# Kernel optimization log

Measured on AMD Instinct MI355X. Metric: run time of the kernel, lower is better.

Reference implementation:

```python
import jax, jax.numpy as jnp
import numpy as np

H = 16        # num_heads
D = 128       # head_dim = hidden_size // num_heads
HID = 2048    # hidden_size
BLOCK = 64    # moba_chunk_size
TOPK = 8      # moba_topk


def setup_inputs() -> dict:
    key = jax.random.key(0)
    ks = jax.random.split(key, 5)
    B, S = 1, 2048
    hidden_states = jax.random.normal(ks[0], (B, S, HID), dtype=jnp.float32)
    scale = HID ** -0.5
    Wq = jax.random.normal(ks[1], (HID, H * D), dtype=jnp.float32) * scale
    Wk = jax.random.normal(ks[2], (HID, H * D), dtype=jnp.float32) * scale
    Wv = jax.random.normal(ks[3], (HID, H * D), dtype=jnp.float32) * scale
    Wo = jax.random.normal(ks[4], (H * D, HID), dtype=jnp.float32) * scale
    return {"hidden_states": hidden_states, "Wq": Wq, "Wk": Wk, "Wv": Wv, "Wo": Wo}


def _moba_forward(hidden_states, Wq, Wk, Wv, Wo):
    B, S, _ = hidden_states.shape
    nb = S // BLOCK
    INF = jnp.float32(jnp.inf)

    q = (hidden_states @ Wq).reshape(B, S, H, D)
    k = (hidden_states @ Wk).reshape(B, S, H, D)
    v = (hidden_states @ Wv).reshape(B, S, H, D)

    # MoBA gating: mean-pooled key per block -> [B, nb, H, D]
    kg = k.reshape(B, nb, BLOCK, H, D).mean(axis=2)
    gate = jnp.einsum('bshd,bnhd->bhsn', q, kg)  # [B,H,S,nb]

    pos = jnp.arange(S)
    qb = pos // BLOCK                 # query's own block
    blk = jnp.arange(nb)
    is_self = qb[:, None] == blk[None, :]                      # self block always selected
    not_past = pos[:, None] < (blk[None, :] + 1) * BLOCK       # blocks not fully in the past
    gate = jnp.where(is_self, INF, jnp.where(not_past, -INF, gate))

    kk = min(TOPK, nb)
    topv, topi = jax.lax.top_k(gate, kk)                       # [B,H,S,kk]
    thresh = topv.min(axis=-1, keepdims=True)
    idx_mask = (topi[..., None] == blk).any(axis=-2)           # [B,H,S,nb]
    need = (gate >= thresh) & idx_mask
    gate_bias = jnp.where(need, 0.0, -INF)                     # additive block mask

    sm_scale = D ** -0.5
    qk = jnp.einsum('bshd,bthd->bhst', q, k) * sm_scale        # [B,H,S,S]
    qk = qk.reshape(B, H, S, nb, BLOCK) + gate_bias[..., None]
    qk = qk.reshape(B, H, S, S)
    causal = pos[:, None] >= pos[None, :]
    qk = jnp.where(causal, qk, -INF)

    p = jax.nn.softmax(qk, axis=-1)
    o = jnp.einsum('bhst,bthd->bshd', p, v).reshape(B, S, H * D)
    return o @ Wo


def reference(hidden_states, Wq, Wk, Wv, Wo):
    # Returns (output, attentions=None, past_key_values=None) in the original;
    # only the output tensor matters for correctness.
    return _moba_forward(hidden_states, Wq, Wk, Wv, Wo)
```

## Files before the change

### kernel.cpp

```cpp
#include <hip/hip_runtime.h>
#include <hip/hip_bf16.h>
#include <stdint.h>
#include <stddef.h>


using bh = __bf16;
typedef __bf16 bhx8 __attribute__((ext_vector_type(8)));
typedef __bf16 bhx4 __attribute__((ext_vector_type(4)));
typedef __bf16 bhx2 __attribute__((ext_vector_type(2)));
typedef float  f32x4 __attribute__((ext_vector_type(4)));

#define SEQ   2048
#define HIDN  2048
#define NHEAD 16
#define HDIM  128
#define NBLK  32
#define BLKSZ 64
#define NQKV  6144
#define NGATE 512
#define LDC   136
#define PSTRIDE ((size_t)SEQ * NGATE)
#define POMSTRIDE 8320

#define GLDS16(gsrc, ldst)                                                     \
  __builtin_amdgcn_global_load_lds(                                            \
      (const __attribute__((address_space(1))) uint32_t*)(gsrc),               \
      (__attribute__((address_space(3))) uint32_t*)(ldst), 16, 0, 0)

__global__ __launch_bounds__(256) void prep(const float* __restrict__ hs,
                                            bh* __restrict__ hs_hi, bh* __restrict__ hs_lo,
                                            const float* __restrict__ Wq, const float* __restrict__ Wk,
                                            const float* __restrict__ Wv, const float* __restrict__ Wo,
                                            bh* __restrict__ wqkvT, bh* __restrict__ woT,
                                            float* __restrict__ hsm) {
  __shared__ float tile[64][33];
  const int b = blockIdx.x;
  const int t = threadIdx.x;
  if (b < 8192) {
    const int z = b >> 11;
    const int b2 = b & 2047;
    const int r0 = (b2 >> 6) * 64, c0 = (b2 & 63) * 32;
    const float* in = (z == 0) ? Wq : (z == 1) ? Wk : (z == 2) ? Wv : Wo;
    bh* out = (z < 3) ? (wqkvT + (size_t)z * HIDN * HIDN) : woT;
#pragma unroll
    for (int it = 0; it < 8; it++) {
      int i = it * 256 + t;
      int row = i >> 5, col = i & 31;
      tile[row][col] = in[(size_t)(r0 + row) * HIDN + c0 + col];
    }
    __syncthreads();
#pragma unroll
    for (int it = 0; it < 4; it++) {
      int i = it * 256 + t;
      int j = i >> 5, p = i & 31;
      bhx2 v2;
      v2[0] = (bh)tile[2 * p][j];
      v2[1] = (bh)tile[2 * p + 1][j];
      *(bhx2*)(out + (size_t)(c0 + j) * HIDN + r0 + 2 * p) = v2;
    }
  } else if (b < 12288) {
    int i = ((b - 8192) * 256 + t) * 4;
    float4 v = *(const float4*)(hs + i);
    bhx4 h4, l4;
    float vv[4] = {v.x, v.y, v.z, v.w};
#pragma unroll
    for (int e = 0; e < 4; e++) {
      bh h = (bh)vv[e];
      h4[e] = h;
      l4[e] = (bh)(vv[e] - (float)h);
    }
    *(bhx4*)(hs_hi + i) = h4;
    *(bhx4*)(hs_lo + i) = l4;
  } else {
    int idx = (b - 12288) * 256 + t;
    int n = idx >> 11, c = idx & 2047;
    const float* p = hs + (size_t)(n * BLKSZ) * HIDN + c;
    float s = 0.f;
#pragma unroll 8
    for (int r = 0; r < BLKSZ; r++) s += p[(size_t)r * HIDN];
    hsm[idx] = s * (1.0f / 64.0f);
  }
}

#define GEMM_STAGE_TILE(SRC, r0_, ldsbase)                                       \
  {                                                                              \
    _Pragma("unroll")                                                            \
    for (int it_ = 0; it_ < 4; it_++) {                                          \
      int idx_ = it_ * 256 + t;                                                  \
      int row_ = idx_ >> 3, x_ = (idx_ & 7) << 4;                                \
      GLDS16((const char*)(SRC) + (size_t)(r0_ + row_) * strideB + kbyte +       \
                 (x_ ^ ((row_ & 7) << 4)),                                       \
             (char*)(ldsbase) + ((idx_ >> 6) << 10));                            \
    }                                                                            \
  }

__global__ __launch_bounds__(256) void qkvkg(const bh* __restrict__ A, const bh* __restrict__ BT,
                                             bh* __restrict__ Cb,
                                             const float* __restrict__ hsm,
                                             const float* __restrict__ Wk,
                                             float* __restrict__ part) {
  __shared__ __align__(16) char smraw[128 * LDC * 2];
  const int t = threadIdx.x;

  if (blockIdx.x < 768) {
    bh* smem = (bh*)smraw;
    bh* As = smem;
    bh* Bs = smem + 128 * 64;
    const int L = t & 63, w = t >> 6;
    const int wm = w & 1, wn = w >> 1;
    const int quad = L >> 4, lo = L & 15;
    const int m0 = (blockIdx.x / 48) * 128, n0 = (blockIdx.x % 48) * 128;
    const size_t strideB = (size_t)HIDN * 2;

    f32x4 acc[4][4];
#pragma unroll
    for (int i = 0; i < 4; i++)
#pragma unroll
      for (int j = 0; j < 4; j++) acc[i][j] = (f32x4){0.f, 0.f, 0.f, 0.f};

    for (int k0 = 0; k0 < HIDN; k0 += 64) {
      const size_t kbyte = (size_t)k0 * 2;
      GEMM_STAGE_TILE(A, m0, As);
      GEMM_STAGE_TILE(BT, n0, Bs);
      __syncthreads();
#pragma unroll
      for (int ks = 0; ks < 2; ks++) {
        bhx8 af[4], bf_[4];
#pragma unroll
        for (int i = 0; i < 4; i++) {
          const int row = wm * 64 + i * 16 + lo;
          af[i] = *(const bhx8*)((const char*)As + row * 128 +
                                 ((ks * 64 + quad * 16) ^ ((row & 7) << 4)));
        }
#pragma unroll
        for (int j = 0; j < 4; j++) {
          const int row = wn * 64 + j * 16 + lo;
          bf_[j] = *(const bhx8*)((const char*)Bs + row * 128 +
                                  ((ks * 64 + quad * 16) ^ ((row & 7) << 4)));
        }
#pragma unroll
        for (int i = 0; i < 4; i++)
#pragma unroll
          for (int j = 0; j < 4; j++)
            acc[i][j] = __builtin_amdgcn_mfma_f32_16x16x32_bf16(af[i], bf_[j], acc[i][j], 0, 0, 0);
      }
      __syncthreads();
    }

    bh* Cs = smem;
#pragma unroll
    for (int i = 0; i < 4; i++)
#pragma unroll
      for (int j = 0; j < 4; j++)
#pragma unroll
        for (int r = 0; r < 4; r++)
          Cs[(wm * 64 + i * 16 + quad * 4 + r) * LDC + wn * 64 + j * 16 + lo] = (bh)acc[i][j][r];
    __syncthreads();
#pragma unroll
    for (int it = 0; it < 8; it++) {
      int idx = it * 256 + t;
      int row = idx >> 4, cg = idx & 15;
      *(uint4*)(Cb + (size_t)(m0 + row) * NQKV + n0 + cg * 8) = *(const uint4*)&Cs[row * LDC + cg * 8];
    }
  } else {
    float (*hl)[32] = (float (*)[32])smraw;
    const int b2 = blockIdx.x - 768;
    const int c = (b2 & 7) * 256 + t;
    const int ky = b2 >> 3;
    const int k0 = ky * 32;
    for (int i = t; i < 32 * 32; i += 256)
      hl[i >> 5][i & 31] = hsm[(size_t)(i >> 5) * HIDN + k0 + (i & 31)];
    __syncthreads();
    float acc[32];
#pragma unroll
    for (int n = 0; n < 32; n++) acc[n] = 0.f;
#pragma unroll 2
    for (int k4 = 0; k4 < 8; k4++) {
      float w0 = Wk[(size_t)(k0 + k4 * 4 + 0) * HIDN + c];
      float w1 = Wk[(size_t)(k0 + k4 * 4 + 1) * HIDN + c];
      float w2 = Wk[(size_t)(k0 + k4 * 4 + 2) * HIDN + c];
      float w3 = Wk[(size_t)(k0 + k4 * 4 + 3) * HIDN + c];
#pragma unroll
      for (int n = 0; n < 32; n++) {
        float4 hv = *(const float4*)&hl[n][k4 * 4];
        acc[n] += hv.x * w0 + hv.y * w1 + hv.z * w2 + hv.w * w3;
      }
    }
#pragma unroll
    for (int n = 0; n < 32; n++)
      part[((size_t)ky * 32 + n) * HIDN + c] = acc[n];
  }
}

__global__ __launch_bounds__(256) void gemm_bt128f(const bh* __restrict__ A, const bh* __restrict__ BT,
                                                   float* __restrict__ Cf, int M, int N, int K) {
  __shared__ __align__(16) bh smem[2 * 128 * 64];
  bh* As = smem;
  bh* Bs = smem + 128 * 64;
  const int t = threadIdx.x;
  const int L = t & 63, w = t >> 6;
  const int wm = w & 1, wn = w >> 1;
  const int quad = L >> 4, lo = L & 15;
  const int m0 = blockIdx.y * 128, n0 = blockIdx.x * 128;
  const size_t strideB = (size_t)K * 2;

  f32x4 acc[4][4];
#pragma unroll
  for (int i = 0; i < 4; i++)
#pragma unroll
    for (int j = 0; j < 4; j++) acc[i][j] = (f32x4){0.f, 0.f, 0.f, 0.f};

  for (int k0 = 0; k0 < K; k0 += 64) {
    const size_t kbyte = (size_t)k0 * 2;
    GEMM_STAGE_TILE(A, m0, As);
    GEMM_STAGE_TILE(BT, n0, Bs);
    __syncthreads();
#pragma unroll
    for (int ks = 0; ks < 2; ks++) {
      bhx8 af[4], bf_[4];
#pragma unroll
      for (int i = 0; i < 4; i++) {
        const int row = wm * 64 + i * 16 + lo;
        af[i] = *(const bhx8*)((const char*)As + row * 128 +
                               ((ks * 64 + quad * 16) ^ ((row & 7) << 4)));
      }
#pragma unroll
      for (int j = 0; j < 4; j++) {
        const int row = wn * 64 + j * 16 + lo;
        bf_[j] = *(const bhx8*)((const char*)Bs + row * 128 +
                                ((ks * 64 + quad * 16) ^ ((row & 7) << 4)));
      }
#pragma unroll
      for (int i = 0; i < 4; i++)
#pragma unroll
        for (int j = 0; j < 4; j++)
          acc[i][j] = __builtin_amdgcn_mfma_f32_16x16x32_bf16(af[i], bf_[j], acc[i][j], 0, 0, 0);
    }
    __syncthreads();
  }

#pragma unroll
  for (int i = 0; i < 4; i++)
#pragma unroll
    for (int j = 0; j < 4; j++)
#pragma unroll
      for (int r = 0; r < 4; r++) {
        int row = m0 + wm * 64 + i * 16 + quad * 4 + r;
        int col = n0 + wn * 64 + j * 16 + lo;
        Cf[(size_t)row * N + col] = acc[i][j][r];
      }
}

__global__ __launch_bounds__(256) void gemm_gate_split(const bh* __restrict__ hs_hi,
                                                       const bh* __restrict__ hs_lo,
                                                       const bh* __restrict__ wg_hi,
                                                       const bh* __restrict__ wg_lo,
                                                       float* __restrict__ part6,
                                                       float* __restrict__ part2) {
  __shared__ __align__(16) bh smem[2 * 128 * 64];
  bh* As = smem;
  bh* Bs = smem + 128 * 64;
  const int t = threadIdx.x;
  const int L = t & 63, w = t >> 6;
  const int wm = w & 1, wn = w >> 1;
  const int quad = L >> 4, lo = L & 15;
  const int t40 = blockIdx.x;
  int cc, mm;
  if (t40 < 16)      { cc = 0; mm = t40; }
  else if (t40 < 28) { cc = 1; mm = t40 - 12; }
  else if (t40 < 36) { cc = 2; mm = t40 - 20; }
  else               { cc = 3; mm = t40 - 24; }
  const int m0 = mm * 128, n0 = cc * 128;
  const int z = blockIdx.z;
  const size_t strideB = (size_t)HIDN * 2;

  f32x4 acc[4][4];
#pragma unroll
  for (int i = 0; i < 4; i++)
#pragma unroll
    for (int j = 0; j < 4; j++) acc[i][j] = (f32x4){0.f, 0.f, 0.f, 0.f};

  for (int k0 = 0; k0 < 768; k0 += 64) {
    const int vk = z * 768 + k0;
    const int ph = vk >> 11;
    const bh* Ap = (ph == 1) ? hs_lo : hs_hi;
    const bh* Bp = (ph == 2) ? wg_lo : wg_hi;
    const size_t kbyte = (size_t)(vk & 2047) * 2;
    GEMM_STAGE_TILE(Ap, m0, As);
    GEMM_STAGE_TILE(Bp, n0, Bs);
    __syncthreads();
#pragma unroll
    for (int ks = 0; ks < 2; ks++) {
      bhx8 af[4], bf_[4];
#pragma unroll
      for (int i = 0; i < 4; i++) {
        const int row = wm * 64 + i * 16 + lo;
        af[i] = *(const bhx8*)((const char*)As + row * 128 +
                               ((ks * 64 + quad * 16) ^ ((row & 7) << 4)));
      }
#pragma unroll
      for (int j = 0; j < 4; j++) {
        const int row = wn * 64 + j * 16 + lo;
        bf_[j] = *(const bhx8*)((const char*)Bs + row * 128 +
                                ((ks * 64 + quad * 16) ^ ((row & 7) << 4)));
      }
#pragma unroll
      for (int i = 0; i < 4; i++)
#pragma unroll
        for (int j = 0; j < 4; j++)
          acc[i][j] = __builtin_amdgcn_mfma_f32_16x16x32_bf16(af[i], bf_[j], acc[i][j], 0, 0, 0);
    }
    __syncthreads();
  }

  float* outp = (z < 6) ? (part6 + (size_t)z * PSTRIDE) : (part2 + (size_t)(z - 6) * PSTRIDE);
#pragma unroll
  for (int i = 0; i < 4; i++)
#pragma unroll
    for (int j = 0; j < 4; j++)
#pragma unroll
      for (int r = 0; r < 4; r++) {
        int row = m0 + wm * 64 + i * 16 + quad * 4 + r;
        int col = n0 + wn * 64 + j * 16 + lo;
        outp[(size_t)row * NGATE + col] = acc[i][j][r];
      }
}

__global__ __launch_bounds__(256) void kg_reduce64(const float* __restrict__ part, float* __restrict__ kg) {
  int idx = blockIdx.x * 256 + threadIdx.x;
  float s = 0.f;
#pragma unroll
  for (int kc = 0; kc < 64; kc++) s += part[(size_t)kc * 65536 + idx];
  kg[idx] = s;
}

__global__ __launch_bounds__(256) void wgk_vtrans(const float* __restrict__ Wq,
                                                  const float* __restrict__ kg,
                                                  bh* __restrict__ wg_hi, bh* __restrict__ wg_lo,
                                                  const bh* __restrict__ qkv, bh* __restrict__ vt) {
  __shared__ __align__(16) char smraw[49792];
  const int b = blockIdx.x;
  const int t = threadIdx.x;
  if (b < 2048) {
    float (*tile)[33] = (float (*)[33])smraw;
    const int h = b >> 7;
    const int b2 = b & 127;
    const int s0 = (b2 >> 2) * 64, d0 = (b2 & 3) * 32;
#pragma unroll
    for (int it = 0; it < 8; it++) {
      int i = it * 256 + t;
      int row = i >> 5, col = i & 31;
      tile[row][col] = (float)qkv[(size_t)(s0 + row) * NQKV + 2 * HIDN + h * HDIM + d0 + col];
    }
    __syncthreads();
#pragma unroll
    for (int it = 0; it < 4; it++) {
      int i = it * 256 + t;
      int j = i >> 5, p = i & 31;
      bhx2 v2;
      v2[0] = (bh)tile[2 * p][j];
      v2[1] = (bh)tile[2 * p + 1][j];
      *(bhx2*)(vt + ((size_t)h * HDIM + d0 + j) * SEQ + s0 + 2 * p) = v2;
    }
  } else {
    float (*wst)[65] = (float (*)[65])smraw;
    float (*kl)[129] = (float (*)[129])(smraw + 33280);
    const int b2 = b - 2048;
    const int h = b2 >> 3;
    const int r0 = (b2 & 7) * 256;
    const int rloc = t & 63, ng = t >> 6;

    for (int i = t; i < 32 * 128; i += 256)
      kl[i >> 7][i & 127] = kg[(size_t)(i >> 7) * HIDN + h * HDIM + (i & 127)];

#pragma unroll
    for (int rt = 0; rt < 4; rt++) {
      __syncthreads();
      for (int i = t; i < 64 * 128; i += 256) {
        int row = i >> 7, col = i & 127;
        wst[col][row] = Wq[(size_t)(r0 + rt * 64 + row) * HIDN + h * HDIM + col];
      }
      __syncthreads();
      float acc8[8];
#pragma unroll
      for (int nn = 0; nn < 8; nn++) acc8[nn] = 0.f;
      for (int d = 0; d < 128; d++) {
        float wv = wst[d][rloc];
#pragma unroll
        for (int nn = 0; nn < 8; nn++)
          acc8[nn] += wv * kl[ng * 8 + nn][d];
      }
#pragma unroll
      for (int nn = 0; nn < 8; nn++) {
        int n = ng * 8 + nn;
        float v = acc8[nn];
        bh hi = (bh)v;
        size_t off = (size_t)(n * 16 + h) * HIDN + r0 + rt * 64 + rloc;
        wg_hi[off] = hi;
        wg_lo[off] = (bh)(v - (float)hi);
      }
    }
  }
}

__global__ __launch_bounds__(256) void gate_topk(const float* __restrict__ part6,
                                                 const float* __restrict__ part2,
                                                 unsigned* __restrict__ bsel) {
  __shared__ float gl[32][17];
  const int s = blockIdx.x;
  const int t = threadIdx.x;
  const int qb = s >> 6;
#pragma unroll
  for (int it = 0; it < 2; it++) {
    int c = it * 256 + t;
    size_t off = (size_t)s * NGATE + c;
    float g = part6[off] + part6[off + PSTRIDE] + part6[off + 2 * PSTRIDE] +
              part6[off + 3 * PSTRIDE] + part6[off + 4 * PSTRIDE] + part6[off + 5 * PSTRIDE] +
              part2[off] + part2[off + PSTRIDE];
    gl[c >> 4][c & 15] = g;
  }
  __syncthreads();
  const int w = t >> 6, L = t & 63;
  const int n = L;
#pragma unroll
  for (int k = 0; k < 4; k++) {
    int h = w * 4 + k;
    float g = -1e30f;
    if (n == qb) g = 1e30f;
    else if (n < qb) g = gl[n][h];
    int rank = 0;
#pragma unroll
    for (int j = 0; j < 32; j++) {
      float gj = __shfl(g, j, 64);
      if (gj > g || (gj == g && j < n)) rank++;
    }
    bool sel = (n <= qb) && (n < 32) && (rank < 8);
    unsigned long long bm = __ballot(sel);
    if (L == 0) bsel[h * SEQ + s] = (unsigned)(bm & 0xffffffffull);
  }
}

__global__ __launch_bounds__(256) void attn(const bh* __restrict__ qkv, const bh* __restrict__ vt,
                                            const unsigned* __restrict__ bsel, bh* __restrict__ obuf,
                                            float* __restrict__ pom) {
  __shared__ __align__(16) bh Ksm[64 * 128];
  __shared__ __align__(16) bh Vsm[128 * 64];
  __shared__ __align__(16) bh PLb[4][16 * 72];
  __shared__ unsigned ublk;
  const int t = threadIdx.x;
  const int w = t >> 6, L = t & 63;
  const int quad = L >> 4, lo = L & 15;
  const int bid = blockIdx.x;
  const int jj = bid >> 3;
  const int h = ((bid & 7) << 1) | (jj & 1);
  const int il = jj >> 1;
  const int i16 = il & 15, grp = il >> 4;
  const int actual = (grp == 0) ? i16 : (grp == 1) ? (31 - i16) : (32 + i16);
  int qb, nlo, nhi, part;
  bool split;
  if (actual < 16)      { qb = actual + 16; part = 1; nlo = 16; nhi = qb; split = true; }
  else if (actual < 32) { qb = actual - 16; part = 0; nlo = 0;  nhi = qb; split = false; }
  else                  { qb = actual - 16; part = 0; nlo = 0;  nhi = 15; split = true; }
  const unsigned wmask = ((nhi == 31) ? 0xFFFFFFFFu : ((1u << (nhi + 1)) - 1)) &
                         (0xFFFFFFFFu << nlo);
  const int s0 = qb * 64 + w * 16;

  unsigned bs[4];
#pragma unroll
  for (int r = 0; r < 4; r++) bs[r] = bsel[h * SEQ + s0 + quad * 4 + r] & wmask;
  unsigned uni = bs[0] | bs[1] | bs[2] | bs[3];
  uni |= (unsigned)__shfl_xor((int)uni, 16);
  uni |= (unsigned)__shfl_xor((int)uni, 32);
  const unsigned uniw = uni;
  if (t == 0) ublk = 0;
  __syncthreads();
  if (L == 0) atomicOr(&ublk, uni);
  __syncthreads();
  const unsigned un = ublk;

  bhx8 aq[4];
  const bh* qrow = qkv + (size_t)(s0 + lo) * NQKV + h * HDIM;
#pragma unroll
  for (int ks = 0; ks < 4; ks++) aq[ks] = *(const bhx8*)(qrow + ks * 32 + quad * 8);

  f32x4 oacc[8];
#pragma unroll
  for (int j = 0; j < 8; j++) oacc[j] = (f32x4){0.f, 0.f, 0.f, 0.f};
  f32x4 lacc = (f32x4){0.f, 0.f, 0.f, 0.f};
  float mi[4] = {-1e30f, -1e30f, -1e30f, -1e30f};

  bhx8 ones8;
#pragma unroll
  for (int e = 0; e < 8; e++) ones8[e] = (bh)1.0f;

  const float scale = 0.08838834764831845f;

  unsigned rem = un;
  while (rem) {
    const int ncur = (int)__builtin_ctz(rem);
    rem &= rem - 1;

    {
      const char* ksrc = (const char*)(qkv + (size_t)(ncur * BLKSZ) * NQKV + HIDN + h * HDIM);
      const char* vsrc = (const char*)(vt + ((size_t)h * HDIM) * SEQ + ncur * BLKSZ);
#pragma unroll
      for (int it = 0; it < 4; it++) {
        int idx = it * 256 + t;
        int row = idx >> 4, x = (idx & 15) << 4;
        GLDS16(ksrc + (size_t)row * (NQKV * 2) + (x ^ ((row & 7) << 4)),
               (char*)Ksm + ((idx >> 6) << 10));
      }
#pragma unroll
      for (int it = 0; it < 4; it++) {
        int idx = it * 256 + t;
        int row = idx >> 3, x = (idx & 7) << 4;
        GLDS16(vsrc + (size_t)row * (SEQ * 2) + (x ^ ((row & 7) << 4)),
               (char*)Vsm + ((idx >> 6) << 10));
      }
    }
    __syncthreads();

    if ((uniw >> ncur) & 1) {
      const char* Kc = (const char*)Ksm;
      const char* Vc = (const char*)Vsm;
      const bool self = (ncur == qb);

      f32x4 sc[4];
      __builtin_amdgcn_s_setprio(1);
#pragma unroll
      for (int nt = 0; nt < 4; nt++) {
        f32x4 s4 = (f32x4){0.f, 0.f, 0.f, 0.f};
#pragma unroll
        for (int ks = 0; ks < 4; ks++) {
          const int row = nt * 16 + lo;
          bhx8 bk = *(const bhx8*)(Kc + row * 256 + ((ks * 64 + quad * 16) ^ ((row & 7) << 4)));
          s4 = __builtin_amdgcn_mfma_f32_16x16x32_bf16(aq[ks], bk, s4, 0, 0, 0);
        }
        sc[nt] = s4;
      }
      __builtin_amdgcn_s_setprio(0);

      if (self) {
#pragma unroll
        for (int nt = 0; nt < 4; nt++)
#pragma unroll
          for (int r = 0; r < 4; r++) {
            float v = sc[nt][r] * scale;
            int kpos = ncur * BLKSZ + nt * 16 + lo;
            int qpos = s0 + quad * 4 + r;
            bool ok = ((bs[r] >> ncur) & 1) && (kpos <= qpos);
            sc[nt][r] = ok ? v : -1e30f;
          }
      } else {
        float bias[4];
#pragma unroll
        for (int r = 0; r < 4; r++)
          bias[r] = ((bs[r] >> ncur) & 1) ? 0.f : -1e30f;
#pragma unroll
        for (int nt = 0; nt < 4; nt++)
#pragma unroll
          for (int r = 0; r < 4; r++)
            sc[nt][r] = sc[nt][r] * scale + bias[r];
      }
      float rm[4];
#pragma unroll
      for (int r = 0; r < 4; r++)
        rm[r] = fmaxf(fmaxf(sc[0][r], sc[1][r]), fmaxf(sc[2][r], sc[3][r]));
#pragma unroll
      for (int off = 1; off < 16; off <<= 1)
#pragma unroll
        for (int r = 0; r < 4; r++) rm[r] = fmaxf(rm[r], __shfl_xor(rm[r], off));

      bool exceed = (rm[0] > mi[0] + 8.f) || (rm[1] > mi[1] + 8.f) ||
                    (rm[2] > mi[2] + 8.f) || (rm[3] > mi[3] + 8.f);
      if (__any(exceed)) {
        float alpha[4];
#pragma unroll
        for (int r = 0; r < 4; r++) {
          float nm = fmaxf(mi[r], rm[r]);
          alpha[r] = __expf(mi[r] - nm);
          mi[r] = nm;
        }
#pragma unroll
        for (int j = 0; j < 8; j++)
#pragma unroll
          for (int r = 0; r < 4; r++) oacc[j][r] *= alpha[r];
#pragma unroll
        for (int r = 0; r < 4; r++) lacc[r] *= alpha[r];
      }

#pragma unroll
      for (int nt = 0; nt < 4; nt++)
#pragma unroll
        for (int r = 0; r < 4; r++) {
          float pv = __expf(sc[nt][r] - mi[r]);
          PLb[w][(quad * 4 + r) * 72 + nt * 16 + lo] = (bh)pv;
        }

      __builtin_amdgcn_s_setprio(1);
#pragma unroll
      for (int kk = 0; kk < 2; kk++) {
        bhx8 pa = *(const bhx8*)&PLb[w][lo * 72 + kk * 32 + quad * 8];
        lacc = __builtin_amdgcn_mfma_f32_16x16x32_bf16(pa, ones8, lacc, 0, 0, 0);
#pragma unroll
        for (int j = 0; j < 8; j++) {
          const int row = j * 16 + lo;
          bhx8 vv = *(const bhx8*)(Vc + row * 128 + ((kk * 64 + quad * 16) ^ ((row & 7) << 4)));
          oacc[j] = __builtin_amdgcn_mfma_f32_16x16x32_bf16(pa, vv, oacc[j], 0, 0, 0);
        }
      }
      __builtin_amdgcn_s_setprio(0);
    }

    __syncthreads();
  }

  if (!split) {
#pragma unroll
    for (int j = 0; j < 8; j++)
#pragma unroll
      for (int r = 0; r < 4; r++) {
        int row = s0 + quad * 4 + r;
        int col = h * HDIM + j * 16 + lo;
        obuf[(size_t)row * HIDN + col] = (bh)(oacc[j][r] / lacc[r]);
      }
  } else {
    float* slab = pom + (size_t)((h * 16 + (qb - 16)) * 2 + part) * POMSTRIDE;
    const int rl0 = w * 16 + quad * 4;
#pragma unroll
    for (int j = 0; j < 8; j++)
#pragma unroll
      for (int r = 0; r < 4; r++)
        slab[(rl0 + r) * 128 + j * 16 + lo] = oacc[j][r];
    if (lo == 0) {
#pragma unroll
      for (int r = 0; r < 4; r++) {
        slab[8192 + rl0 + r] = mi[r];
        slab[8256 + rl0 + r] = lacc[r];
      }
    }
  }
}

__global__ __launch_bounds__(256) void attn_combine(const float* __restrict__ pom,
                                                    bh* __restrict__ obuf) {
  const int b = blockIdx.x;
  const int h = b >> 4, qs = b & 15;
  const int t = threadIdx.x;
  const float* s0 = pom + (size_t)((h * 16 + qs) * 2 + 0) * POMSTRIDE;
  const float* s1 = s0 + POMSTRIDE;
  const int rl = t >> 2;
  const int c0 = (t & 3) * 32;
  float m0 = s0[8192 + rl], l0 = s0[8256 + rl];
  float m1 = s1[8192 + rl], l1 = s1[8256 + rl];
  float m = fmaxf(m0, m1);
  float a0 = __expf(m0 - m), a1 = __expf(m1 - m);
  float inv = 1.f / (l0 * a0 + l1 * a1);
  a0 *= inv; a1 *= inv;
  const int row = (qs + 16) * 64 + rl;
  bh* orow = obuf + (size_t)row * HIDN + h * HDIM + c0;
  const float* p0 = s0 + rl * 128 + c0;
  const float* p1 = s1 + rl * 128 + c0;
#pragma unroll
  for (int c = 0; c < 32; c += 4) {
    float4 v0 = *(const float4*)(p0 + c);
    float4 v1 = *(const float4*)(p1 + c);
    bhx4 o4;
    o4[0] = (bh)(v0.x * a0 + v1.x * a1);
    o4[1] = (bh)(v0.y * a0 + v1.y * a1);
    o4[2] = (bh)(v0.z * a0 + v1.z * a1);
    o4[3] = (bh)(v0.w * a0 + v1.w * a1);
    *(bhx4*)(orow + c) = o4;
  }
}

extern "C" void kernel_launch(void* const* d_in, const int* in_sizes, int n_in,
                              void* d_out, int out_size, void* d_ws, size_t ws_size,
                              hipStream_t stream) {
  const float* hs = (const float*)d_in[0];
  const float* Wq = (const float*)d_in[1];
  const float* Wk = (const float*)d_in[2];
  const float* Wv = (const float*)d_in[3];
  const float* Wo = (const float*)d_in[4];

  char* ws = (char*)d_ws;
  bh* hs_hi = (bh*)ws;            ws += (size_t)SEQ * HIDN * 2;
  bh* hs_lo = (bh*)ws;            ws += (size_t)SEQ * HIDN * 2;
  bh* wqkvT = (bh*)ws;            ws += (size_t)NQKV * HIDN * 2;
  bh* woT = (bh*)ws;              ws += (size_t)HIDN * HIDN * 2;
  bh* qkv = (bh*)ws;              ws += (size_t)SEQ * NQKV * 2;
  bh* vt = (bh*)ws;               ws += (size_t)NHEAD * HDIM * SEQ * 2;
  bh* obuf = (bh*)ws;             ws += (size_t)SEQ * HIDN * 2;
  float* hsm = (float*)ws;        ws += (size_t)NBLK * HIDN * 4;
  float* kg = (float*)ws;         ws += (size_t)NBLK * HIDN * 4;
  bh* wg_hi = (bh*)ws;            ws += (size_t)NGATE * HIDN * 2;
  bh* wg_lo = (bh*)ws;            ws += (size_t)NGATE * HIDN * 2;
  unsigned* bsel = (unsigned*)ws; ws += (size_t)NHEAD * SEQ * 4;
  float* kg_part = (float*)vt;
  float* gpart6 = (float*)wqkvT;
  float* gpart2 = (float*)obuf;
  float* pom = (float*)wqkvT;

  prep<<<8192 + 4096 + 256, 256, 0, stream>>>(hs, hs_hi, hs_lo, Wq, Wk, Wv, Wo, wqkvT, woT, hsm);

  qkvkg<<<768 + 512, 256, 0, stream>>>(hs_hi, wqkvT, qkv, hsm, Wk, kg_part);

  kg_reduce64<<<(NBLK * HIDN) / 256, 256, 0, stream>>>(kg_part, kg);
  wgk_vtrans<<<2048 + 128, 256, 0, stream>>>(Wq, kg, wg_hi, wg_lo, qkv, vt);
  gemm_gate_split<<<dim3(40, 1, 8), 256, 0, stream>>>(
      hs_hi, hs_lo, wg_hi, wg_lo, gpart6, gpart2);
  gate_topk<<<SEQ, 256, 0, stream>>>(gpart6, gpart2, bsel);

  attn<<<768, 256, 0, stream>>>(qkv, vt, bsel, obuf, pom);
  attn_combine<<<256, 256, 0, stream>>>(pom, obuf);

  gemm_bt128f<<<dim3(HIDN / 128, SEQ / 128), 256, 0, stream>>>(obuf, woT, (float*)d_out, SEQ, HIDN, HIDN);
}
```

Baseline: 411.2 us.

## Rewrite QKV GEMM with 256x192 tiles, double-buffered LDS and 512 threads

The fused QKV projection GEMM now uses 512-thread blocks computing 256x192 output tiles. Two 56 KB LDS buffers in dynamic shared memory let the next K-slice prefetch be interleaved with MFMA phases, with s_setprio raising priority around the MFMA bursts. The kg-partial side job is regrouped so each block handles four K-chunks, keeping the grid at 64+256 blocks. The aim is better data reuse and overlap of loads with compute, at the cost of fewer, heavier blocks (256 GEMM blocks) and high LDS use per block.

```diff
diff --git a/kernel.cpp b/kernel.cpp
--- a/kernel.cpp
+++ b/kernel.cpp
@@ -21,6 +21,8 @@
 #define LDC   136
 #define PSTRIDE ((size_t)SEQ * NGATE)
 #define POMSTRIDE 8320
+#define QBUF  57344
+#define QLDS  (2 * QBUF)
 
 #define GLDS16(gsrc, ldst)                                                     \
   __builtin_amdgcn_global_load_lds(                                            \
@@ -94,101 +96,166 @@
     }                                                                            \
   }
 
-__global__ __launch_bounds__(256) void qkvkg(const bh* __restrict__ A, const bh* __restrict__ BT,
+__global__ __launch_bounds__(512) void qkvkg(const bh* __restrict__ A, const bh* __restrict__ BT,
                                              bh* __restrict__ Cb,
                                              const float* __restrict__ hsm,
                                              const float* __restrict__ Wk,
                                              float* __restrict__ part) {
-  __shared__ __align__(16) char smraw[128 * LDC * 2];
+  extern __shared__ __align__(16) char dynsm[];
   const int t = threadIdx.x;
 
-  if (blockIdx.x < 768) {
-    bh* smem = (bh*)smraw;
-    bh* As = smem;
-    bh* Bs = smem + 128 * 64;
-    const int L = t & 63, w = t >> 6;
-    const int wm = w & 1, wn = w >> 1;
+  if (blockIdx.x >= 64) {
+    const int tid2 = blockIdx.x - 64;
+    const int m0 = (tid2 >> 5) * 256, n0 = (tid2 & 31) * 192;
+    const int wave = t >> 6, L = t & 63;
+    const int wm = wave >> 2, wn = wave & 3;
     const int quad = L >> 4, lo = L & 15;
-    const int m0 = (blockIdx.x / 48) * 128, n0 = (blockIdx.x % 48) * 128;
-    const size_t strideB = (size_t)HIDN * 2;
-
-    f32x4 acc[4][4];
-#pragma unroll
-    for (int i = 0; i < 4; i++)
-#pragma unroll
-      for (int j = 0; j < 4; j++) acc[i][j] = (f32x4){0.f, 0.f, 0.f, 0.f};
-
-    for (int k0 = 0; k0 < HIDN; k0 += 64) {
-      const size_t kbyte = (size_t)k0 * 2;
-      GEMM_STAGE_TILE(A, m0, As);
-      GEMM_STAGE_TILE(BT, n0, Bs);
+
+    f32x4 acc[8][3];
+#pragma unroll
+    for (int i = 0; i < 8; i++)
+#pragma unroll
+      for (int j = 0; j < 3; j++) acc[i][j] = (f32x4){0.f, 0.f, 0.f, 0.f};
+
+    auto stage_round = [&](int nb, int r, size_t kbyte) {
+      int idx = r * 512 + t;
+      const char* src;
+      if (idx < 2048) {
+        int row = idx >> 3, x = (idx & 7) << 4;
+        src = (const char*)A + (size_t)(m0 + row) * (HIDN * 2) + kbyte + (x ^ ((row & 7) << 4));
+      } else {
+        int j = idx - 2048;
+        int row = j >> 3, x = (j & 7) << 4;
+        src = (const char*)BT + (size_t)(n0 + row) * (HIDN * 2) + kbyte + (x ^ ((row & 7) << 4));
+      }
+      GLDS16(src, dynsm + nb * QBUF + ((idx >> 6) << 10));
+    };
+
+#define AFRAG(Ab, mi, ks)                                                       \
+  (*(const bhx8*)((Ab) + (size_t)(wm * 128 + (mi) * 16 + lo) * 128 +            \
+                  (((ks) * 64 + quad * 16) ^ ((lo & 7) << 4))))
+#define BFRAG(Bb, ni, ks)                                                       \
+  (*(const bhx8*)((Bb) + (size_t)(wn * 48 + (ni) * 16 + lo) * 128 +             \
+                  (((ks) * 64 + quad * 16) ^ ((lo & 7) << 4))))
+#define QPHASE(p, a00, a01, a10, a11)                                           \
+  {                                                                             \
+    __builtin_amdgcn_s_setprio(1);                                              \
+    acc[2*(p)][0] = __builtin_amdgcn_mfma_f32_16x16x32_bf16(a00, b00, acc[2*(p)][0], 0, 0, 0);   \
+    acc[2*(p)][0] = __builtin_amdgcn_mfma_f32_16x16x32_bf16(a01, b01, acc[2*(p)][0], 0, 0, 0);   \
+    acc[2*(p)][1] = __builtin_amdgcn_mfma_f32_16x16x32_bf16(a00, b10, acc[2*(p)][1], 0, 0, 0);   \
+    acc[2*(p)][1] = __builtin_amdgcn_mfma_f32_16x16x32_bf16(a01, b11, acc[2*(p)][1], 0, 0, 0);   \
+    acc[2*(p)][2] = __builtin_amdgcn_mfma_f32_16x16x32_bf16(a00, b20, acc[2*(p)][2], 0, 0, 0);   \
+    acc[2*(p)][2] = __builtin_amdgcn_mfma_f32_16x16x32_bf16(a01, b21, acc[2*(p)][2], 0, 0, 0);   \
+    acc[2*(p)+1][0] = __builtin_amdgcn_mfma_f32_16x16x32_bf16(a10, b00, acc[2*(p)+1][0], 0, 0, 0); \
+    acc[2*(p)+1][0] = __builtin_amdgcn_mfma_f32_16x16x32_bf16(a11, b01, acc[2*(p)+1][0], 0, 0, 0); \
+    acc[2*(p)+1][1] = __builtin_amdgcn_mfma_f32_16x16x32_bf16(a10, b10, acc[2*(p)+1][1], 0, 0, 0); \
+    acc[2*(p)+1][1] = __builtin_amdgcn_mfma_f32_16x16x32_bf16(a11, b11, acc[2*(p)+1][1], 0, 0, 0); \
+    acc[2*(p)+1][2] = __builtin_amdgcn_mfma_f32_16x16x32_bf16(a10, b20, acc[2*(p)+1][2], 0, 0, 0); \
+    acc[2*(p)+1][2] = __builtin_amdgcn_mfma_f32_16x16x32_bf16(a11, b21, acc[2*(p)+1][2], 0, 0, 0); \
+    __builtin_amdgcn_s_setprio(0);                                              \
+  }
+
+#pragma unroll
+    for (int r = 0; r < 7; r++) stage_round(0, r, 0);
+    asm volatile("s_waitcnt vmcnt(0)" ::: "memory");
+    __builtin_amdgcn_s_barrier();
+
+    for (int tk = 0; tk < 32; ++tk) {
+      const int cur = tk & 1;
+      const char* Ab = dynsm + cur * QBUF;
+      const char* Bb = Ab + 32768;
+      const int nb = cur ^ 1;
+      const size_t kb1 = (size_t)(tk + 1) * 128;
+      const bool pf = (tk + 1) < 32;
+
+      if (pf) { stage_round(nb, 0, kb1); stage_round(nb, 1, kb1); }
+      bhx8 b00 = BFRAG(Bb, 0, 0), b01 = BFRAG(Bb, 0, 1);
+      bhx8 b10 = BFRAG(Bb, 1, 0), b11 = BFRAG(Bb, 1, 1);
+      bhx8 b20 = BFRAG(Bb, 2, 0), b21 = BFRAG(Bb, 2, 1);
+      {
+        bhx8 a00 = AFRAG(Ab, 0, 0), a01 = AFRAG(Ab, 0, 1);
+        bhx8 a10 = AFRAG(Ab, 1, 0), a11 = AFRAG(Ab, 1, 1);
+        QPHASE(0, a00, a01, a10, a11);
+      }
+      if (pf) { stage_round(nb, 2, kb1); stage_round(nb, 3, kb1); }
+      {
+        bhx8 a00 = AFRAG(Ab, 2, 0), a01 = AFRAG(Ab, 2, 1);
+        bhx8 a10 = AFRAG(Ab, 3, 0), a11 = AFRAG(Ab, 3, 1);
+        QPHASE(1, a00, a01, a10, a11);
+      }
+      if (pf) { stage_round(nb, 4, kb1); stage_round(nb, 5, kb1); }
+      {
+        bhx8 a00 = AFRAG(Ab, 4, 0), a01 = AFRAG(Ab, 4, 1);
+        bhx8 a10 = AFRAG(Ab, 5, 0), a11 = AFRAG(Ab, 5, 1);
+        QPHASE(2, a00, a01, a10, a11);
+      }
+      if (pf) { stage_round(nb, 6, kb1); }
+      {
+        bhx8 a00 = AFRAG(Ab, 6, 0), a01 = AFRAG(Ab, 6, 1);
+        bhx8 a10 = AFRAG(Ab, 7, 0), a11 = AFRAG(Ab, 7, 1);
+        QPHASE(3, a00, a01, a10, a11);
+      }
+      asm volatile("s_waitcnt vmcnt(0)" ::: "memory");
+      __builtin_amdgcn_s_barrier();
+    }
+
+    bh* Cs = (bh*)dynsm;
+#pragma unroll
+    for (int hh = 0; hh < 2; ++hh) {
+      if (wm == hh) {
+#pragma unroll
+        for (int mi = 0; mi < 8; mi++)
+#pragma unroll
+          for (int ni = 0; ni < 3; ni++)
+#pragma unroll
+            for (int r = 0; r < 4; r++)
+              Cs[(mi * 16 + quad * 4 + r) * 200 + wn * 48 + ni * 16 + lo] = (bh)acc[mi][ni][r];
+      }
       __syncthreads();
 #pragma unroll
-      for (int ks = 0; ks < 2; ks++) {
-        bhx8 af[4], bf_[4];
-#pragma unroll
-        for (int i = 0; i < 4; i++) {
-          const int row = wm * 64 + i * 16 + lo;
-          af[i] = *(const bhx8*)((const char*)As + row * 128 +
-                                 ((ks * 64 + quad * 16) ^ ((row & 7) << 4)));
+      for (int rr = 0; rr < 6; rr++) {
+        int idx = rr * 512 + t;
+        int row = idx / 24, cg = idx % 24;
+        *(uint4*)(Cb + (size_t)(m0 + hh * 128 + row) * NQKV + n0 + cg * 8) =
+            *(const uint4*)&Cs[row * 200 + cg * 8];
+      }
+      __syncthreads();
+    }
+#undef AFRAG
+#undef BFRAG
+#undef QPHASE
+  } else {
+    float (*hl)[32] = (float (*)[32])dynsm;
+    const int b2 = blockIdx.x;
+    const int c = (b2 & 3) * 512 + t;
+    const int kyg = b2 >> 2;
+#pragma unroll
+    for (int g = 0; g < 4; g++) {
+      const int ky = kyg * 4 + g;
+      const int k0 = ky * 32;
+      __syncthreads();
+      for (int i = t; i < 32 * 32; i += 512)
+        hl[i >> 5][i & 31] = hsm[(size_t)(i >> 5) * HIDN + k0 + (i & 31)];
+      __syncthreads();
+      float acc[32];
+#pragma unroll
+      for (int n = 0; n < 32; n++) acc[n] = 0.f;
+#pragma unroll 2
+      for (int k4 = 0; k4 < 8; k4++) {
+        float w0 = Wk[(size_t)(k0 + k4 * 4 + 0) * HIDN + c];
+        float w1 = Wk[(size_t)(k0 + k4 * 4 + 1) * HIDN + c];
+        float w2 = Wk[(size_t)(k0 + k4 * 4 + 2) * HIDN + c];
+        float w3 = Wk[(size_t)(k0 + k4 * 4 + 3) * HIDN + c];
+#pragma unroll
+        for (int n = 0; n < 32; n++) {
+          float4 hv = *(const float4*)&hl[n][k4 * 4];
+          acc[n] += hv.x * w0 + hv.y * w1 + hv.z * w2 + hv.w * w3;
         }
-#pragma unroll
-        for (int j = 0; j < 4; j++) {
-          const int row = wn * 64 + j * 16 + lo;
-          bf_[j] = *(const bhx8*)((const char*)Bs + row * 128 +
-                                  ((ks * 64 + quad * 16) ^ ((row & 7) << 4)));
-        }
-#pragma unroll
-        for (int i = 0; i < 4; i++)
-#pragma unroll
-          for (int j = 0; j < 4; j++)
-            acc[i][j] = __builtin_amdgcn_mfma_f32_16x16x32_bf16(af[i], bf_[j], acc[i][j], 0, 0, 0);
-      }
-      __syncthreads();
-    }
-
-    bh* Cs = smem;
-#pragma unroll
-    for (int i = 0; i < 4; i++)
-#pragma unroll
-      for (int j = 0; j < 4; j++)
-#pragma unroll
-        for (int r = 0; r < 4; r++)
-          Cs[(wm * 64 + i * 16 + quad * 4 + r) * LDC + wn * 64 + j * 16 + lo] = (bh)acc[i][j][r];
-    __syncthreads();
-#pragma unroll
-    for (int it = 0; it < 8; it++) {
-      int idx = it * 256 + t;
-      int row = idx >> 4, cg = idx & 15;
-      *(uint4*)(Cb + (size_t)(m0 + row) * NQKV + n0 + cg * 8) = *(const uint4*)&Cs[row * LDC + cg * 8];
-    }
-  } else {
-    float (*hl)[32] = (float (*)[32])smraw;
-    const int b2 = blockIdx.x - 768;
-    const int c = (b2 & 7) * 256 + t;
-    const int ky = b2 >> 3;
-    const int k0 = ky * 32;
-    for (int i = t; i < 32 * 32; i += 256)
-      hl[i >> 5][i & 31] = hsm[(size_t)(i >> 5) * HIDN + k0 + (i & 31)];
-    __syncthreads();
-    float acc[32];
-#pragma unroll
-    for (int n = 0; n < 32; n++) acc[n] = 0.f;
-#pragma unroll 2
-    for (int k4 = 0; k4 < 8; k4++) {
-      float w0 = Wk[(size_t)(k0 + k4 * 4 + 0) * HIDN + c];
-      float w1 = Wk[(size_t)(k0 + k4 * 4 + 1) * HIDN + c];
-      float w2 = Wk[(size_t)(k0 + k4 * 4 + 2) * HIDN + c];
-      float w3 = Wk[(size_t)(k0 + k4 * 4 + 3) * HIDN + c];
-#pragma unroll
-      for (int n = 0; n < 32; n++) {
-        float4 hv = *(const float4*)&hl[n][k4 * 4];
-        acc[n] += hv.x * w0 + hv.y * w1 + hv.z * w2 + hv.w * w3;
-      }
-    }
-#pragma unroll
-    for (int n = 0; n < 32; n++)
-      part[((size_t)ky * 32 + n) * HIDN + c] = acc[n];
+      }
+#pragma unroll
+      for (int n = 0; n < 32; n++)
+        part[((size_t)ky * 32 + n) * HIDN + c] = acc[n];
+    }
   }
 }
 
@@ -703,7 +770,7 @@
 
   prep<<<8192 + 4096 + 256, 256, 0, stream>>>(hs, hs_hi, hs_lo, Wq, Wk, Wv, Wo, wqkvT, woT, hsm);
 
-  qkvkg<<<768 + 512, 256, 0, stream>>>(hs_hi, wqkvT, qkv, hsm, Wk, kg_part);
+  qkvkg<<<64 + 256, 512, QLDS, stream>>>(hs_hi, wqkvT, qkv, hsm, Wk, kg_part);
 
   kg_reduce64<<<(NBLK * HIDN) / 256, 256, 0, stream>>>(kg_part, kg);
   wgk_vtrans<<<2048 + 128, 256, 0, stream>>>(Wq, kg, wg_hi, wg_lo, qkv, vt);
```

New measurement: 420.7 us. 2.3% more time.
